# Kernel tuning notes

Measured on AMD Instinct MI355X. Metric: run time of the kernel, lower is better.

The kernel has to match this reference:

```python
import jax, jax.numpy as jnp
import numpy as np

B, T, C = 2, 2048, 1024
H = 16
HD = C // H  # head_dim = 64
SCALE = HD ** -0.5

def setup_inputs() -> dict:
    key = jax.random.key(0)
    ks = jax.random.split(key, 5)
    s = 1.0 / np.sqrt(C)
    return {
        "x": jax.random.normal(ks[0], (B, T, C), dtype=jnp.float32),
        "Wq": jax.random.normal(ks[1], (C, C), dtype=jnp.float32) * s,
        "Wk": jax.random.normal(ks[2], (C, C), dtype=jnp.float32) * s,
        "Wv": jax.random.normal(ks[3], (C, C), dtype=jnp.float32) * s,
        "Wp": jax.random.normal(ks[4], (C, C), dtype=jnp.float32) * s,
        "bp": jnp.zeros((C,), dtype=jnp.float32),
    }

def reference(x, Wq, Wk, Wv, Wp, bp):
    b, t, c = x.shape
    # QKV projections (no bias, qkv_bias=False) -> [B,T,H,HD]
    q = (x @ Wq).reshape(b, t, H, HD)
    k = (x @ Wk).reshape(b, t, H, HD)
    v = (x @ Wv).reshape(b, t, H, HD)
    # scores [B,H,T,T]
    scores = jnp.einsum("bqhd,bkhd->bhqk", q, k) * SCALE
    causal = jnp.tril(jnp.ones((t, t), dtype=bool))
    scores = jnp.where(causal, scores, -jnp.inf)
    attn = jax.nn.softmax(scores, axis=-1)  # dropout = identity (eval mode)
    out = jnp.einsum("bhqk,bkhd->bqhd", attn, v).reshape(b, t, c)
    return out @ Wp + bp
```

## Files before the change

### kernel.cpp

```cpp
#include <hip/hip_runtime.h>


typedef __attribute__((ext_vector_type(8))) short shortx8;
typedef __attribute__((ext_vector_type(4))) short shortx4;
typedef __attribute__((ext_vector_type(8))) unsigned short ushortx8;
typedef __attribute__((ext_vector_type(4))) float f32x4;
typedef __attribute__((ext_vector_type(16))) float f32x16;
typedef __attribute__((ext_vector_type(2))) unsigned uintx2;

#define MFMA16(a, b, c) __builtin_amdgcn_mfma_f32_16x16x32_bf16((a), (b), (c), 0, 0, 0)
#define MFMA32(a, b, c) __builtin_amdgcn_mfma_f32_32x32x16_bf16((a), (b), (c), 0, 0, 0)

#define SC_L2E 0.18033688011112042f

__device__ __forceinline__ unsigned short f2bf(float f) {
  union { float f; unsigned u; } v; v.f = f;
  unsigned r = v.u + 0x7fffu + ((v.u >> 16) & 1u);
  return (unsigned short)(r >> 16);
}

__device__ __forceinline__ unsigned cvtpk(float a, float b) {
  unsigned r;
  asm("v_cvt_pk_bf16_f32 %0, %1, %2" : "=v"(r) : "v"(a), "v"(b));
  return r;
}

__device__ __forceinline__ float fexp2(float x) {
#if __has_builtin(__builtin_amdgcn_exp2f)
  return __builtin_amdgcn_exp2f(x);
#else
  return exp2f(x);
#endif
}

__device__ __forceinline__ uintx2 plswap(unsigned a, unsigned b) {
#if __has_builtin(__builtin_amdgcn_permlane32_swap)
  return __builtin_amdgcn_permlane32_swap(a, b, false, false);
#else
  asm volatile("v_permlane32_swap_b32 %0, %1" : "+v"(a), "+v"(b));
  uintx2 r; r[0] = a; r[1] = b; return r;
#endif
}

__device__ __forceinline__ float partner32(float x, int hi) {
  unsigned u = __builtin_bit_cast(unsigned, x);
  uintx2 r = plswap(u, u);
  return __builtin_bit_cast(float, hi ? r[0] : r[1]);
}

__device__ __forceinline__ float max3(float a, float b, float c) {
  return fmaxf(fmaxf(a, b), c);
}

__device__ __forceinline__ void gload16(const void* g, void* l) {
  __builtin_amdgcn_global_load_lds(
      (const __attribute__((address_space(1))) void*)g,
      (__attribute__((address_space(3))) void*)l, 16, 0, 0);
}

__global__ __launch_bounds__(256) void cvt_x(const float* __restrict__ x,
                                             unsigned short* __restrict__ xb, int n4) {
  int i = blockIdx.x * 256 + threadIdx.x;
  if (i < n4) {
    float4 v = ((const float4*)x)[i];
    unsigned short* o = xb + (size_t)i * 4;
    o[0] = f2bf(v.x); o[1] = f2bf(v.y); o[2] = f2bf(v.z); o[3] = f2bf(v.w);
  }
}

__global__ __launch_bounds__(256) void transpose_w4(
    const float* __restrict__ Wq, const float* __restrict__ Wk,
    const float* __restrict__ Wv, const float* __restrict__ Wp,
    unsigned short* __restrict__ wqkvT, unsigned short* __restrict__ wpT) {
  __shared__ float tile[32][33];
  const int zi = blockIdx.z;
  const float* src = (zi == 0) ? Wq : (zi == 1) ? Wk : (zi == 2) ? Wv : Wp;
  unsigned short* dst = (zi == 3) ? wpT : wqkvT + (size_t)zi * 1048576;
  const int bx = blockIdx.x * 32, by = blockIdx.y * 32;
  const int tx = threadIdx.x & 31, ty = threadIdx.x >> 5;
  #pragma unroll
  for (int i = 0; i < 32; i += 8)
    tile[ty + i][tx] = src[(size_t)(by + ty + i) * 1024 + bx + tx];
  __syncthreads();
  #pragma unroll
  for (int i = 0; i < 32; i += 8)
    dst[(size_t)(bx + ty + i) * 1024 + by + tx] = f2bf(tile[tx][ty + i]);
}

__global__ __launch_bounds__(256) void gemm_bt(
    const unsigned short* __restrict__ A, const unsigned short* __restrict__ BT,
    unsigned short* __restrict__ Cb, float* __restrict__ Cf,
    const float* __restrict__ bias, int M, int N, int K,
    float qscale, int scale_cols, unsigned short* __restrict__ vTo) {
  __shared__ unsigned short As[3][4096];
  __shared__ unsigned short Bs[3][4096];
  const int tid = threadIdx.x;
  const int lane = tid & 63, w = tid >> 6;
  const int wr = w >> 1, wc = w & 1;
  const int brow = blockIdx.y << 7, bcol = blockIdx.x << 7;

  f32x4 z = {0.f, 0.f, 0.f, 0.f};
  f32x4 acc[4][4];
  #pragma unroll
  for (int m = 0; m < 4; ++m)
    #pragma unroll
    for (int n = 0; n < 4; ++n) acc[m][n] = z;

  const int srow = tid >> 2;
  const int scol = (tid & 3) << 3;
  const unsigned short* Ap = A + (size_t)(brow + srow) * K + scol;
  const unsigned short* Bp = BT + (size_t)(bcol + srow) * K + scol;
  const size_t rowK64 = (size_t)64 * K;

  #define GSTAGE(k0_, bi_)                                   \
    do {                                                     \
      unsigned short* AsW = &As[bi_][w * 512];               \
      unsigned short* BsW = &Bs[bi_][w * 512];               \
      gload16(Ap + (k0_), AsW);                              \
      gload16(Ap + rowK64 + (k0_), AsW + 2048);              \
      gload16(Bp + (k0_), BsW);                              \
      gload16(Bp + rowK64 + (k0_), BsW + 2048);              \
    } while (0)

  const int koff = (lane >> 4) << 3;
  const int ar = (wr << 6) + (lane & 15);
  const int br = (wc << 6) + (lane & 15);
  const int nt = K >> 5;
  int cur = 0;
  GSTAGE(0, 0);
  for (int t = 0; t < nt; ++t) {
    const int nxt = (cur + 1 == 3) ? 0 : cur + 1;
    if (t + 1 < nt) {
      GSTAGE((size_t)(t + 1) << 5, nxt);
      asm volatile("s_waitcnt vmcnt(4)" ::: "memory");
    } else {
      asm volatile("s_waitcnt vmcnt(0)" ::: "memory");
    }
    __builtin_amdgcn_sched_barrier(0);
    __builtin_amdgcn_s_barrier();
    __builtin_amdgcn_sched_barrier(0);
    shortx8 af[4], bf[4];
    #pragma unroll
    for (int m = 0; m < 4; ++m) af[m] = *(const shortx8*)&As[cur][(ar + m * 16) * 32 + koff];
    #pragma unroll
    for (int n = 0; n < 4; ++n) bf[n] = *(const shortx8*)&Bs[cur][(br + n * 16) * 32 + koff];
    #pragma unroll
    for (int m = 0; m < 4; ++m)
      #pragma unroll
      for (int n = 0; n < 4; ++n) acc[m][n] = MFMA16(af[m], bf[n], acc[m][n]);
    asm volatile("s_waitcnt lgkmcnt(0)" ::: "memory");
    __builtin_amdgcn_sched_barrier(0);
    cur = nxt;
  }
  #undef GSTAGE

  const int r0 = (lane >> 4) << 2;
  const int c0 = lane & 15;
  if (Cb) {
    if (vTo && bcol >= 2048) {
      #pragma unroll
      for (int m = 0; m < 4; ++m)
        #pragma unroll
        for (int n = 0; n < 4; ++n) {
          const int dp = bcol - 2048 + (wc << 6) + n * 16 + c0;
          const size_t rowb = brow + (wr << 6) + m * 16 + r0;
          uint2 u;
          u.x = cvtpk(acc[m][n][0], acc[m][n][1]);
          u.y = cvtpk(acc[m][n][2], acc[m][n][3]);
          *(uint2*)&vTo[(size_t)dp * 4096 + rowb] = u;
        }
    } else {
      #pragma unroll
      for (int m = 0; m < 4; ++m)
        #pragma unroll
        for (int n = 0; n < 4; ++n)
          #pragma unroll
          for (int j = 0; j < 4; ++j) {
            const size_t row = brow + (wr << 6) + m * 16 + r0 + j;
            const size_t col = bcol + (wc << 6) + n * 16 + c0;
            float v = acc[m][n][j];
            if ((int)col < scale_cols) v *= qscale;
            Cb[row * N + col] = f2bf(v);
          }
    }
  } else {
    #pragma unroll
    for (int m = 0; m < 4; ++m)
      #pragma unroll
      for (int n = 0; n < 4; ++n)
        #pragma unroll
        for (int j = 0; j < 4; ++j) {
          const size_t row = brow + (wr << 6) + m * 16 + r0 + j;
          const size_t col = bcol + (wc << 6) + n * 16 + c0;
          Cf[row * N + col] = acc[m][n][j] + bias[col];
        }
  }
}


__global__ __launch_bounds__(256, 4) void attn_fwd(
    const unsigned short* __restrict__ qkv, const unsigned short* __restrict__ vT,
    unsigned short* __restrict__ att) {
  __shared__ unsigned short sh[4][4096];

  const int tid = threadIdx.x;
  const int lane = tid & 63;
  const int p = tid >> 6;
  const int stream = blockIdx.x;
  const int h = stream & 15, b = stream >> 4;
  const int qb = 63 - (int)blockIdx.y;
  const int ql = lane & 31;
  const int hi = lane >> 5;
  const int q = qb * 32 + ql;

  shortx8 qf[4];
  {
    const unsigned short* qp = qkv + ((size_t)(b * 2048 + q)) * 3072 + h * 64 + 8 * hi;
    #pragma unroll
    for (int kc = 0; kc < 4; ++kc) qf[kc] = *(const shortx8*)(qp + 16 * kc);
  }

  f32x16 z16;
  #pragma unroll
  for (int i = 0; i < 16; ++i) z16[i] = 0.f;
  f32x16 accO0 = z16, accO1 = z16;
  float m_run = -__builtin_inff(), l_run = 0.f;

  const unsigned short* kb[4];
  const unsigned short* vb[4];
  #pragma unroll
  for (int i = 0; i < 4; ++i) {
    const int krow = 8 * i + (lane >> 3);
    const int kcl = (lane & 7) ^ (((krow >> 1) ^ (krow >> 4)) & 7);
    kb[i] = qkv + ((size_t)(b * 2048 + krow)) * 3072 + 1024 + h * 64 + 8 * kcl;
    const int vrow = 16 * i + (lane >> 2);
    const int vcl = (lane & 3) ^ (((vrow >> 1) ^ (vrow >> 3)) & 3);
    vb[i] = vT + ((size_t)(h * 64 + vrow)) * 4096 + b * 2048 + 8 * vcl;
  }
  const int rs8 = ((ql >> 1) ^ (ql >> 4)) & 7;
  const int rs4 = ((ql >> 1) ^ (ql >> 3)) & 3;

  unsigned short* Kl = &sh[p][0];
  unsigned short* Vl = &sh[p][2048];

  #define STAGE(t_)                                                        \
    do {                                                                   \
      _Pragma("unroll")                                                    \
      for (int i = 0; i < 4; ++i)                                          \
        gload16(kb[i] + (size_t)(t_) * 32 * 3072, Kl + i * 512);           \
      _Pragma("unroll")                                                    \
      for (int i = 0; i < 4; ++i)                                          \
        gload16(vb[i] + (t_) * 32, Vl + i * 512);                          \
    } while (0)

  if (p <= qb) STAGE(p);
  for (int t = p; t <= qb; t += 4) {
    asm volatile("s_waitcnt vmcnt(4)" ::: "memory");
    __builtin_amdgcn_sched_barrier(0);
    shortx8 kf[4];
    #pragma unroll
    for (int kc = 0; kc < 4; ++kc)
      kf[kc] = *(const shortx8*)&Kl[ql * 64 + 8 * ((2 * kc + hi) ^ rs8)];
    asm volatile("s_waitcnt lgkmcnt(0)" ::: "memory");
    __builtin_amdgcn_sched_barrier(0);

    __builtin_amdgcn_s_setprio(1);
    f32x16 s = z16;
    #pragma unroll
    for (int kc = 0; kc < 4; ++kc) s = MFMA32(kf[kc], qf[kc], s);
    __builtin_amdgcn_s_setprio(0);

    asm volatile("s_waitcnt vmcnt(0)" ::: "memory");
    __builtin_amdgcn_sched_barrier(0);
    shortx8 vf[2][2];
    #pragma unroll
    for (int dh = 0; dh < 2; ++dh)
      #pragma unroll
      for (int ks = 0; ks < 2; ++ks)
        vf[dh][ks] = *(const shortx8*)&Vl[(32 * dh + ql) * 32 + 8 * ((2 * ks + hi) ^ rs4)];
    asm volatile("s_waitcnt lgkmcnt(0)" ::: "memory");
    __builtin_amdgcn_sched_barrier(0);

    if (t + 4 <= qb) STAGE(t + 4);

    if (t == qb) {
      #pragma unroll
      for (int r = 0; r < 16; ++r) {
        const int kvl = (r & 3) + 8 * (r >> 2) + 4 * hi;
        if (kvl > ql) s[r] = -__builtin_inff();
      }
    }

    float t0 = max3(s[0], s[1], s[2]);
    float t1 = max3(s[3], s[4], s[5]);
    float t2 = max3(s[6], s[7], s[8]);
    float t3 = max3(s[9], s[10], s[11]);
    float t4 = max3(s[12], s[13], s[14]);
    float mx = fmaxf(max3(t0, t1, t2), max3(t3, t4, s[15]));
    mx = fmaxf(mx, partner32(mx, hi));

    if (!__all(mx <= m_run + 8.0f)) {
      const float nm = fmaxf(m_run, mx);
      const float alpha = fexp2(m_run - nm);
      l_run *= alpha;
      #pragma unroll
      for (int r = 0; r < 16; ++r) { accO0[r] *= alpha; accO1[r] *= alpha; }
      m_run = nm;
    }

    #pragma unroll
    for (int r = 0; r < 16; ++r) s[r] = fexp2(s[r] - m_run);
    float a8[8], a4[4];
    #pragma unroll
    for (int i = 0; i < 8; ++i) a8[i] = s[2 * i] + s[2 * i + 1];
    #pragma unroll
    for (int i = 0; i < 4; ++i) a4[i] = a8[2 * i] + a8[2 * i + 1];
    float rsum = (a4[0] + a4[1]) + (a4[2] + a4[3]);
    rsum += partner32(rsum, hi);
    l_run += rsum;

    unsigned wv[8];
    #pragma unroll
    for (int i = 0; i < 8; ++i) wv[i] = cvtpk(s[2 * i], s[2 * i + 1]);
    __builtin_amdgcn_s_setprio(1);
    #pragma unroll
    for (int ss = 0; ss < 2; ++ss) {
      uintx2 r02 = plswap(wv[4 * ss], wv[4 * ss + 2]);
      uintx2 r13 = plswap(wv[4 * ss + 1], wv[4 * ss + 3]);
      union { unsigned u[4]; shortx8 s8; } pb;
      pb.u[0] = r02[0];
      pb.u[1] = r13[0];
      pb.u[2] = r02[1];
      pb.u[3] = r13[1];
      accO0 = MFMA32(vf[0][ss], pb.s8, accO0);
      accO1 = MFMA32(vf[1][ss], pb.s8, accO1);
    }
    __builtin_amdgcn_s_setprio(0);
  }
  #undef STAGE

  float* fb = (float*)&sh[0][0];
  #define DUMP(slot_)                                                          \
    do {                                                                       \
      float* ob = fb + (slot_) * 2048;                                         \
      _Pragma("unroll")                                                        \
      for (int rg = 0; rg < 4; ++rg) {                                         \
        f32x4 v0 = {accO0[4 * rg], accO0[4 * rg + 1],                          \
                    accO0[4 * rg + 2], accO0[4 * rg + 3]};                     \
        f32x4 v1 = {accO1[4 * rg], accO1[4 * rg + 1],                          \
                    accO1[4 * rg + 2], accO1[4 * rg + 3]};                     \
        *(f32x4*)&ob[(rg * 64 + lane) * 4] = v0;                               \
        *(f32x4*)&ob[((4 + rg) * 64 + lane) * 4] = v1;                         \
      }                                                                        \
      fb[4096 + (slot_) * 128 + lane] = m_run;                                 \
      fb[4096 + (slot_) * 128 + 64 + lane] = l_run;                            \
    } while (0)
  #define MERGE(slot_)                                                         \
    do {                                                                       \
      const float m2 = fb[4096 + (slot_) * 128 + lane];                        \
      const float l2 = fb[4096 + (slot_) * 128 + 64 + lane];                   \
      if (m2 != -__builtin_inff()) {                                           \
        float* ob = fb + (slot_) * 2048;                                       \
        const float mf = fmaxf(m_run, m2);                                     \
        const float a1 = fexp2(m_run - mf);                                    \
        const float a2 = fexp2(m2 - mf);                                       \
        _Pragma("unroll")                                                      \
        for (int rg = 0; rg < 4; ++rg) {                                       \
          f32x4 p0 = *(const f32x4*)&ob[(rg * 64 + lane) * 4];                 \
          f32x4 p1 = *(const f32x4*)&ob[((4 + rg) * 64 + lane) * 4];           \
          _Pragma("unroll")                                                    \
          for (int j = 0; j < 4; ++j) {                                        \
            accO0[4 * rg + j] = accO0[4 * rg + j] * a1 + p0[j] * a2;           \
            accO1[4 * rg + j] = accO1[4 * rg + j] * a1 + p1[j] * a2;           \
          }                                                                    \
        }                                                                      \
        l_run = l_run * a1 + l2 * a2;                                          \
        m_run = mf;                                                            \
      }                                                                        \
    } while (0)

  __syncthreads();
  if (p == 1) DUMP(0);
  if (p == 3) DUMP(1);
  __syncthreads();
  if (p == 0) MERGE(0);
  if (p == 2) MERGE(1);
  __syncthreads();
  if (p == 2) DUMP(0);
  __syncthreads();
  if (p == 0) {
    MERGE(0);
    const float inv = 1.f / l_run;
    unsigned short* op = att + ((size_t)(b * 2048 + q)) * 1024 + h * 64;
    #pragma unroll
    for (int rq = 0; rq < 4; ++rq) {
      shortx4 o0, o1;
      #pragma unroll
      for (int j = 0; j < 4; ++j) {
        o0[j] = (short)f2bf(accO0[4 * rq + j] * inv);
        o1[j] = (short)f2bf(accO1[4 * rq + j] * inv);
      }
      *(shortx4*)&op[8 * rq + 4 * hi] = o0;
      *(shortx4*)&op[32 + 8 * rq + 4 * hi] = o1;
    }
  }
  #undef DUMP
  #undef MERGE
}

extern "C" void kernel_launch(void* const* d_in, const int* in_sizes, int n_in,
                              void* d_out, int out_size, void* d_ws, size_t ws_size,
                              hipStream_t stream) {
  const float* x  = (const float*)d_in[0];
  const float* Wq = (const float*)d_in[1];
  const float* Wk = (const float*)d_in[2];
  const float* Wv = (const float*)d_in[3];
  const float* Wp = (const float*)d_in[4];
  const float* bp = (const float*)d_in[5];

  char* ws = (char*)d_ws;
  unsigned short* xb    = (unsigned short*)(ws);
  unsigned short* wqkvT = (unsigned short*)(ws + (size_t)8  * 1048576);
  unsigned short* wpT   = (unsigned short*)(ws + (size_t)14 * 1048576);
  unsigned short* qkv   = (unsigned short*)(ws + (size_t)16 * 1048576);
  unsigned short* vT    = (unsigned short*)(ws + (size_t)40 * 1048576);
  unsigned short* att   = (unsigned short*)(ws + (size_t)48 * 1048576);

  cvt_x<<<dim3(4096), dim3(256), 0, stream>>>(x, xb, 1048576);
  transpose_w4<<<dim3(32, 32, 4), dim3(256), 0, stream>>>(Wq, Wk, Wv, Wp, wqkvT, wpT);
  gemm_bt<<<dim3(24, 32), dim3(256), 0, stream>>>(xb, wqkvT, qkv, nullptr, nullptr,
                                                  4096, 3072, 1024, SC_L2E, 1024, vT);
  attn_fwd<<<dim3(32, 64), dim3(256), 0, stream>>>(qkv, vT, att);
  gemm_bt<<<dim3(8, 32), dim3(256), 0, stream>>>(att, wpT, nullptr, (float*)d_out, bp,
                                                 4096, 1024, 1024, 0.f, 0, nullptr);
}
```

Before: 107.8 us.

## Shrink GEMM blocks to 128x64 tiles with two waves and double buffering

The bf16 GEMM changes from 128x128 tiles computed by four waves to 128x64 tiles computed by two waves. This doubles the grid for both the QKV and output projections, and the smaller output-projection launch gains more blocks to spread across CUs. The LDS pipeline drops from triple to double buffering, with an extra barrier per k-step so a buffer is not overwritten while still being read. The trade-off is less operand reuse per block, more global traffic for the A operand, and extra synchronisation per k-step.

```diff
diff --git a/kernel.cpp b/kernel.cpp
--- a/kernel.cpp
+++ b/kernel.cpp
@@ -87,17 +87,16 @@
     dst[(size_t)(bx + ty + i) * 1024 + by + tx] = f2bf(tile[tx][ty + i]);
 }
 
-__global__ __launch_bounds__(256) void gemm_bt(
+__global__ __launch_bounds__(128) void gemm_bt(
     const unsigned short* __restrict__ A, const unsigned short* __restrict__ BT,
     unsigned short* __restrict__ Cb, float* __restrict__ Cf,
     const float* __restrict__ bias, int M, int N, int K,
     float qscale, int scale_cols, unsigned short* __restrict__ vTo) {
-  __shared__ unsigned short As[3][4096];
-  __shared__ unsigned short Bs[3][4096];
+  __shared__ unsigned short As[2][4096];
+  __shared__ unsigned short Bs[2][2048];
   const int tid = threadIdx.x;
   const int lane = tid & 63, w = tid >> 6;
-  const int wr = w >> 1, wc = w & 1;
-  const int brow = blockIdx.y << 7, bcol = blockIdx.x << 7;
+  const int brow = blockIdx.y << 7, bcol = blockIdx.x << 6;
 
   f32x4 z = {0.f, 0.f, 0.f, 0.f};
   f32x4 acc[4][4];
@@ -110,29 +109,30 @@
   const int scol = (tid & 3) << 3;
   const unsigned short* Ap = A + (size_t)(brow + srow) * K + scol;
   const unsigned short* Bp = BT + (size_t)(bcol + srow) * K + scol;
-  const size_t rowK64 = (size_t)64 * K;
-
-  #define GSTAGE(k0_, bi_)                                   \
-    do {                                                     \
-      unsigned short* AsW = &As[bi_][w * 512];               \
-      unsigned short* BsW = &Bs[bi_][w * 512];               \
-      gload16(Ap + (k0_), AsW);                              \
-      gload16(Ap + rowK64 + (k0_), AsW + 2048);              \
-      gload16(Bp + (k0_), BsW);                              \
-      gload16(Bp + rowK64 + (k0_), BsW + 2048);              \
+  const size_t rowK32 = (size_t)32 * K;
+
+  #define GSTAGE(k0_, bi_)                                            \
+    do {                                                              \
+      _Pragma("unroll")                                               \
+      for (int i = 0; i < 4; ++i)                                     \
+        gload16(Ap + (size_t)i * rowK32 + (k0_),                      \
+                &As[bi_][i * 1024 + (w << 9)]);                       \
+      _Pragma("unroll")                                               \
+      for (int i = 0; i < 2; ++i)                                     \
+        gload16(Bp + (size_t)i * rowK32 + (k0_),                      \
+                &Bs[bi_][i * 1024 + (w << 9)]);                       \
     } while (0)
 
   const int koff = (lane >> 4) << 3;
-  const int ar = (wr << 6) + (lane & 15);
-  const int br = (wc << 6) + (lane & 15);
+  const int ar = (w << 6) + (lane & 15);
+  const int br = (lane & 15);
   const int nt = K >> 5;
-  int cur = 0;
+  int bufi = 0;
   GSTAGE(0, 0);
   for (int t = 0; t < nt; ++t) {
-    const int nxt = (cur + 1 == 3) ? 0 : cur + 1;
     if (t + 1 < nt) {
-      GSTAGE((size_t)(t + 1) << 5, nxt);
-      asm volatile("s_waitcnt vmcnt(4)" ::: "memory");
+      GSTAGE((size_t)(t + 1) << 5, bufi ^ 1);
+      asm volatile("s_waitcnt vmcnt(6)" ::: "memory");
     } else {
       asm volatile("s_waitcnt vmcnt(0)" ::: "memory");
     }
@@ -141,16 +141,18 @@
     __builtin_amdgcn_sched_barrier(0);
     shortx8 af[4], bf[4];
     #pragma unroll
-    for (int m = 0; m < 4; ++m) af[m] = *(const shortx8*)&As[cur][(ar + m * 16) * 32 + koff];
-    #pragma unroll
-    for (int n = 0; n < 4; ++n) bf[n] = *(const shortx8*)&Bs[cur][(br + n * 16) * 32 + koff];
+    for (int m = 0; m < 4; ++m) af[m] = *(const shortx8*)&As[bufi][(ar + m * 16) * 32 + koff];
+    #pragma unroll
+    for (int n = 0; n < 4; ++n) bf[n] = *(const shortx8*)&Bs[bufi][(br + n * 16) * 32 + koff];
     #pragma unroll
     for (int m = 0; m < 4; ++m)
       #pragma unroll
       for (int n = 0; n < 4; ++n) acc[m][n] = MFMA16(af[m], bf[n], acc[m][n]);
     asm volatile("s_waitcnt lgkmcnt(0)" ::: "memory");
     __builtin_amdgcn_sched_barrier(0);
-    cur = nxt;
+    __builtin_amdgcn_s_barrier();
+    __builtin_amdgcn_sched_barrier(0);
+    bufi ^= 1;
   }
   #undef GSTAGE
 
@@ -162,8 +164,8 @@
       for (int m = 0; m < 4; ++m)
         #pragma unroll
         for (int n = 0; n < 4; ++n) {
-          const int dp = bcol - 2048 + (wc << 6) + n * 16 + c0;
-          const size_t rowb = brow + (wr << 6) + m * 16 + r0;
+          const int dp = bcol - 2048 + n * 16 + c0;
+          const size_t rowb = brow + (w << 6) + m * 16 + r0;
           uint2 u;
           u.x = cvtpk(acc[m][n][0], acc[m][n][1]);
           u.y = cvtpk(acc[m][n][2], acc[m][n][3]);
@@ -176,8 +178,8 @@
         for (int n = 0; n < 4; ++n)
           #pragma unroll
           for (int j = 0; j < 4; ++j) {
-            const size_t row = brow + (wr << 6) + m * 16 + r0 + j;
-            const size_t col = bcol + (wc << 6) + n * 16 + c0;
+            const size_t row = brow + (w << 6) + m * 16 + r0 + j;
+            const size_t col = bcol + n * 16 + c0;
             float v = acc[m][n][j];
             if ((int)col < scale_cols) v *= qscale;
             Cb[row * N + col] = f2bf(v);
@@ -190,8 +192,8 @@
       for (int n = 0; n < 4; ++n)
         #pragma unroll
         for (int j = 0; j < 4; ++j) {
-          const size_t row = brow + (wr << 6) + m * 16 + r0 + j;
-          const size_t col = bcol + (wc << 6) + n * 16 + c0;
+          const size_t row = brow + (w << 6) + m * 16 + r0 + j;
+          const size_t col = bcol + n * 16 + c0;
           Cf[row * N + col] = acc[m][n][j] + bias[col];
         }
   }
@@ -428,9 +430,9 @@
 
   cvt_x<<<dim3(4096), dim3(256), 0, stream>>>(x, xb, 1048576);
   transpose_w4<<<dim3(32, 32, 4), dim3(256), 0, stream>>>(Wq, Wk, Wv, Wp, wqkvT, wpT);
-  gemm_bt<<<dim3(24, 32), dim3(256), 0, stream>>>(xb, wqkvT, qkv, nullptr, nullptr,
+  gemm_bt<<<dim3(48, 32), dim3(128), 0, stream>>>(xb, wqkvT, qkv, nullptr, nullptr,
                                                   4096, 3072, 1024, SC_L2E, 1024, vT);
   attn_fwd<<<dim3(32, 64), dim3(256), 0, stream>>>(qkv, vT, att);
-  gemm_bt<<<dim3(8, 32), dim3(256), 0, stream>>>(att, wpT, nullptr, (float*)d_out, bp,
-                                                 4096, 1024, 1024, 0.f, 0, nullptr);
-}
+  gemm_bt<<<dim3(16, 32), dim3(128), 0, stream>>>(att, wpT, nullptr, (float*)d_out, bp,
+                                                  4096, 1024, 1024, 0.f, 0, nullptr);
+}
```

New measurement: 118.7 us. +10.0%, slower.

## Process two 32-row query tiles per attention block to reuse staged K/V

Applied to the files above, without the earlier changes.

Each attention workgroup now handles 64 query rows as two 32-row sub-tiles (A and B) that share every K/V tile staged in LDS, which halves the grid and the global K/V traffic per query. Sub-tile A is skipped on the final KV tile, and each sub-tile gets its own causal mask. Launch bounds drop from 4 to 3 waves per SIMD to make room for the doubled accumulators and Q fragments. The cost is lower occupancy, twice as many cross-wave merge trees at the end, and fewer blocks to balance the causal workload.

```diff
diff --git a/kernel.cpp b/kernel.cpp
--- a/kernel.cpp
+++ b/kernel.cpp
@@ -198,7 +198,7 @@
 }
 
 
-__global__ __launch_bounds__(256, 4) void attn_fwd(
+__global__ __launch_bounds__(256, 3) void attn_fwd(
     const unsigned short* __restrict__ qkv, const unsigned short* __restrict__ vT,
     unsigned short* __restrict__ att) {
   __shared__ unsigned short sh[4][4096];
@@ -208,23 +208,30 @@
   const int p = tid >> 6;
   const int stream = blockIdx.x;
   const int h = stream & 15, b = stream >> 4;
-  const int qb = 63 - (int)blockIdx.y;
+  const int qb = 31 - (int)blockIdx.y;
   const int ql = lane & 31;
   const int hi = lane >> 5;
-  const int q = qb * 32 + ql;
-
-  shortx8 qf[4];
+  const int qA = qb * 64 + ql;
+  const int qB = qA + 32;
+
+  shortx8 qfA[4], qfB[4];
   {
-    const unsigned short* qp = qkv + ((size_t)(b * 2048 + q)) * 3072 + h * 64 + 8 * hi;
-    #pragma unroll
-    for (int kc = 0; kc < 4; ++kc) qf[kc] = *(const shortx8*)(qp + 16 * kc);
+    const unsigned short* qpA = qkv + ((size_t)(b * 2048 + qA)) * 3072 + h * 64 + 8 * hi;
+    const unsigned short* qpB = qkv + ((size_t)(b * 2048 + qB)) * 3072 + h * 64 + 8 * hi;
+    #pragma unroll
+    for (int kc = 0; kc < 4; ++kc) {
+      qfA[kc] = *(const shortx8*)(qpA + 16 * kc);
+      qfB[kc] = *(const shortx8*)(qpB + 16 * kc);
+    }
   }
 
   f32x16 z16;
   #pragma unroll
   for (int i = 0; i < 16; ++i) z16[i] = 0.f;
-  f32x16 accO0 = z16, accO1 = z16;
-  float m_run = -__builtin_inff(), l_run = 0.f;
+  f32x16 accA0 = z16, accA1 = z16;
+  f32x16 accB0 = z16, accB1 = z16;
+  float mA = -__builtin_inff(), lA = 0.f;
+  float mB = -__builtin_inff(), lB = 0.f;
 
   const unsigned short* kb[4];
   const unsigned short* vb[4];
@@ -253,8 +260,57 @@
         gload16(vb[i] + (t_) * 32, Vl + i * 512);                          \
     } while (0)
 
-  if (p <= qb) STAGE(p);
-  for (int t = p; t <= qb; t += 4) {
+  #define SMAX(s_, mr_, lr_, A0_, A1_, wv_)                                \
+    do {                                                                   \
+      float t0 = max3(s_[0], s_[1], s_[2]);                                \
+      float t1 = max3(s_[3], s_[4], s_[5]);                                \
+      float t2 = max3(s_[6], s_[7], s_[8]);                                \
+      float t3 = max3(s_[9], s_[10], s_[11]);                              \
+      float t4 = max3(s_[12], s_[13], s_[14]);                             \
+      float mx = fmaxf(max3(t0, t1, t2), max3(t3, t4, s_[15]));            \
+      mx = fmaxf(mx, partner32(mx, hi));                                   \
+      if (!__all(mx <= (mr_) + 8.0f)) {                                    \
+        const float nm = fmaxf(mr_, mx);                                   \
+        const float alpha = fexp2((mr_) - nm);                             \
+        (lr_) *= alpha;                                                    \
+        _Pragma("unroll")                                                  \
+        for (int r = 0; r < 16; ++r) { A0_[r] *= alpha; A1_[r] *= alpha; } \
+        (mr_) = nm;                                                        \
+      }                                                                    \
+      _Pragma("unroll")                                                    \
+      for (int r = 0; r < 16; ++r) s_[r] = fexp2(s_[r] - (mr_));           \
+      float a8[8], a4[4];                                                  \
+      _Pragma("unroll")                                                    \
+      for (int i = 0; i < 8; ++i) a8[i] = s_[2 * i] + s_[2 * i + 1];       \
+      _Pragma("unroll")                                                    \
+      for (int i = 0; i < 4; ++i) a4[i] = a8[2 * i] + a8[2 * i + 1];       \
+      float rsum = (a4[0] + a4[1]) + (a4[2] + a4[3]);                      \
+      rsum += partner32(rsum, hi);                                         \
+      (lr_) += rsum;                                                       \
+      _Pragma("unroll")                                                    \
+      for (int i = 0; i < 8; ++i) wv_[i] = cvtpk(s_[2 * i], s_[2 * i + 1]);\
+    } while (0)
+
+  #define PV(wv_, A0_, A1_)                                                \
+    do {                                                                   \
+      _Pragma("unroll")                                                    \
+      for (int ss = 0; ss < 2; ++ss) {                                     \
+        uintx2 r02 = plswap(wv_[4 * ss], wv_[4 * ss + 2]);                 \
+        uintx2 r13 = plswap(wv_[4 * ss + 1], wv_[4 * ss + 3]);             \
+        union { unsigned u[4]; shortx8 s8; } pb;                           \
+        pb.u[0] = r02[0];                                                  \
+        pb.u[1] = r13[0];                                                  \
+        pb.u[2] = r02[1];                                                  \
+        pb.u[3] = r13[1];                                                  \
+        A0_ = MFMA32(vf[0][ss], pb.s8, A0_);                               \
+        A1_ = MFMA32(vf[1][ss], pb.s8, A1_);                               \
+      }                                                                    \
+    } while (0)
+
+  const int tmax = 2 * qb + 1;
+  if (p <= tmax) STAGE(p);
+  for (int t = p; t <= tmax; t += 4) {
+    const bool actA = (t <= 2 * qb);
     asm volatile("s_waitcnt vmcnt(4)" ::: "memory");
     __builtin_amdgcn_sched_barrier(0);
     shortx8 kf[4];
@@ -264,10 +320,27 @@
     asm volatile("s_waitcnt lgkmcnt(0)" ::: "memory");
     __builtin_amdgcn_sched_barrier(0);
 
+    unsigned wvA[8];
+    if (actA) {
+      __builtin_amdgcn_s_setprio(1);
+      f32x16 sA = z16;
+      #pragma unroll
+      for (int kc = 0; kc < 4; ++kc) sA = MFMA32(kf[kc], qfA[kc], sA);
+      __builtin_amdgcn_s_setprio(0);
+      if (t == 2 * qb) {
+        #pragma unroll
+        for (int r = 0; r < 16; ++r) {
+          const int kvl = (r & 3) + 8 * (r >> 2) + 4 * hi;
+          if (kvl > ql) sA[r] = -__builtin_inff();
+        }
+      }
+      SMAX(sA, mA, lA, accA0, accA1, wvA);
+    }
+
     __builtin_amdgcn_s_setprio(1);
-    f32x16 s = z16;
-    #pragma unroll
-    for (int kc = 0; kc < 4; ++kc) s = MFMA32(kf[kc], qf[kc], s);
+    f32x16 sB = z16;
+    #pragma unroll
+    for (int kc = 0; kc < 4; ++kc) sB = MFMA32(kf[kc], qfB[kc], sB);
     __builtin_amdgcn_s_setprio(0);
 
     asm volatile("s_waitcnt vmcnt(0)" ::: "memory");
@@ -281,88 +354,47 @@
     asm volatile("s_waitcnt lgkmcnt(0)" ::: "memory");
     __builtin_amdgcn_sched_barrier(0);
 
-    if (t + 4 <= qb) STAGE(t + 4);
-
-    if (t == qb) {
+    if (t + 4 <= tmax) STAGE(t + 4);
+
+    if (t == tmax) {
       #pragma unroll
       for (int r = 0; r < 16; ++r) {
         const int kvl = (r & 3) + 8 * (r >> 2) + 4 * hi;
-        if (kvl > ql) s[r] = -__builtin_inff();
+        if (kvl > ql) sB[r] = -__builtin_inff();
       }
     }
-
-    float t0 = max3(s[0], s[1], s[2]);
-    float t1 = max3(s[3], s[4], s[5]);
-    float t2 = max3(s[6], s[7], s[8]);
-    float t3 = max3(s[9], s[10], s[11]);
-    float t4 = max3(s[12], s[13], s[14]);
-    float mx = fmaxf(max3(t0, t1, t2), max3(t3, t4, s[15]));
-    mx = fmaxf(mx, partner32(mx, hi));
-
-    if (!__all(mx <= m_run + 8.0f)) {
-      const float nm = fmaxf(m_run, mx);
-      const float alpha = fexp2(m_run - nm);
-      l_run *= alpha;
-      #pragma unroll
-      for (int r = 0; r < 16; ++r) { accO0[r] *= alpha; accO1[r] *= alpha; }
-      m_run = nm;
-    }
-
-    #pragma unroll
-    for (int r = 0; r < 16; ++r) s[r] = fexp2(s[r] - m_run);
-    float a8[8], a4[4];
-    #pragma unroll
-    for (int i = 0; i < 8; ++i) a8[i] = s[2 * i] + s[2 * i + 1];
-    #pragma unroll
-    for (int i = 0; i < 4; ++i) a4[i] = a8[2 * i] + a8[2 * i + 1];
-    float rsum = (a4[0] + a4[1]) + (a4[2] + a4[3]);
-    rsum += partner32(rsum, hi);
-    l_run += rsum;
-
-    unsigned wv[8];
-    #pragma unroll
-    for (int i = 0; i < 8; ++i) wv[i] = cvtpk(s[2 * i], s[2 * i + 1]);
+    unsigned wvB[8];
+    SMAX(sB, mB, lB, accB0, accB1, wvB);
+
     __builtin_amdgcn_s_setprio(1);
-    #pragma unroll
-    for (int ss = 0; ss < 2; ++ss) {
-      uintx2 r02 = plswap(wv[4 * ss], wv[4 * ss + 2]);
-      uintx2 r13 = plswap(wv[4 * ss + 1], wv[4 * ss + 3]);
-      union { unsigned u[4]; shortx8 s8; } pb;
-      pb.u[0] = r02[0];
-      pb.u[1] = r13[0];
-      pb.u[2] = r02[1];
-      pb.u[3] = r13[1];
-      accO0 = MFMA32(vf[0][ss], pb.s8, accO0);
-      accO1 = MFMA32(vf[1][ss], pb.s8, accO1);
-    }
+    if (actA) PV(wvA, accA0, accA1);
+    PV(wvB, accB0, accB1);
     __builtin_amdgcn_s_setprio(0);
   }
   #undef STAGE
 
   float* fb = (float*)&sh[0][0];
-  #define DUMP(slot_)                                                          \
+  #define DUMP(slot_, A0_, A1_, mr_, lr_)                                      \
     do {                                                                       \
       float* ob = fb + (slot_) * 2048;                                         \
       _Pragma("unroll")                                                        \
       for (int rg = 0; rg < 4; ++rg) {                                         \
-        f32x4 v0 = {accO0[4 * rg], accO0[4 * rg + 1],                          \
-                    accO0[4 * rg + 2], accO0[4 * rg + 3]};                     \
-        f32x4 v1 = {accO1[4 * rg], accO1[4 * rg + 1],                          \
-                    accO1[4 * rg + 2], accO1[4 * rg + 3]};                     \
+        f32x4 v0 = {A0_[4 * rg], A0_[4 * rg + 1], A0_[4 * rg + 2], A0_[4 * rg + 3]}; \
+        f32x4 v1 = {A1_[4 * rg], A1_[4 * rg + 1], A1_[4 * rg + 2], A1_[4 * rg + 3]}; \
         *(f32x4*)&ob[(rg * 64 + lane) * 4] = v0;                               \
         *(f32x4*)&ob[((4 + rg) * 64 + lane) * 4] = v1;                         \
       }                                                                        \
-      fb[4096 + (slot_) * 128 + lane] = m_run;                                 \
-      fb[4096 + (slot_) * 128 + 64 + lane] = l_run;                            \
-    } while (0)
-  #define MERGE(slot_)                                                         \
+      fb[4096 + (slot_) * 128 + lane] = (mr_);                                 \
+      fb[4096 + (slot_) * 128 + 64 + lane] = (lr_);                            \
+    } while (0)
+  #define MERGE(slot_, A0_, A1_, mr_, lr_)                                     \
     do {                                                                       \
       const float m2 = fb[4096 + (slot_) * 128 + lane];                        \
       const float l2 = fb[4096 + (slot_) * 128 + 64 + lane];                   \
       if (m2 != -__builtin_inff()) {                                           \
         float* ob = fb + (slot_) * 2048;                                       \
-        const float mf = fmaxf(m_run, m2);                                     \
-        const float a1 = fexp2(m_run - mf);                                    \
+        const float mf = fmaxf(mr_, m2);                                       \
+        const float a1 = fexp2((mr_) - mf);                                    \
         const float a2 = fexp2(m2 - mf);                                       \
         _Pragma("unroll")                                                      \
         for (int rg = 0; rg < 4; ++rg) {                                       \
@@ -370,42 +402,50 @@
           f32x4 p1 = *(const f32x4*)&ob[((4 + rg) * 64 + lane) * 4];           \
           _Pragma("unroll")                                                    \
           for (int j = 0; j < 4; ++j) {                                        \
-            accO0[4 * rg + j] = accO0[4 * rg + j] * a1 + p0[j] * a2;           \
-            accO1[4 * rg + j] = accO1[4 * rg + j] * a1 + p1[j] * a2;           \
+            A0_[4 * rg + j] = A0_[4 * rg + j] * a1 + p0[j] * a2;               \
+            A1_[4 * rg + j] = A1_[4 * rg + j] * a1 + p1[j] * a2;               \
           }                                                                    \
         }                                                                      \
-        l_run = l_run * a1 + l2 * a2;                                          \
-        m_run = mf;                                                            \
+        (lr_) = (lr_) * a1 + l2 * a2;                                          \
+        (mr_) = mf;                                                            \
       }                                                                        \
     } while (0)
-
-  __syncthreads();
-  if (p == 1) DUMP(0);
-  if (p == 3) DUMP(1);
-  __syncthreads();
-  if (p == 0) MERGE(0);
-  if (p == 2) MERGE(1);
-  __syncthreads();
-  if (p == 2) DUMP(0);
-  __syncthreads();
-  if (p == 0) {
-    MERGE(0);
-    const float inv = 1.f / l_run;
-    unsigned short* op = att + ((size_t)(b * 2048 + q)) * 1024 + h * 64;
-    #pragma unroll
-    for (int rq = 0; rq < 4; ++rq) {
-      shortx4 o0, o1;
-      #pragma unroll
-      for (int j = 0; j < 4; ++j) {
-        o0[j] = (short)f2bf(accO0[4 * rq + j] * inv);
-        o1[j] = (short)f2bf(accO1[4 * rq + j] * inv);
-      }
-      *(shortx4*)&op[8 * rq + 4 * hi] = o0;
-      *(shortx4*)&op[32 + 8 * rq + 4 * hi] = o1;
-    }
-  }
+  #define TREE(A0_, A1_, mr_, lr_, qrow_)                                      \
+    do {                                                                       \
+      __syncthreads();                                                         \
+      if (p == 1) DUMP(0, A0_, A1_, mr_, lr_);                                 \
+      if (p == 3) DUMP(1, A0_, A1_, mr_, lr_);                                 \
+      __syncthreads();                                                         \
+      if (p == 0) MERGE(0, A0_, A1_, mr_, lr_);                                \
+      if (p == 2) MERGE(1, A0_, A1_, mr_, lr_);                                \
+      __syncthreads();                                                         \
+      if (p == 2) DUMP(0, A0_, A1_, mr_, lr_);                                 \
+      __syncthreads();                                                         \
+      if (p == 0) {                                                            \
+        MERGE(0, A0_, A1_, mr_, lr_);                                          \
+        const float inv = 1.f / (lr_);                                         \
+        unsigned short* op = att + ((size_t)(b * 2048 + (qrow_))) * 1024 + h * 64; \
+        _Pragma("unroll")                                                      \
+        for (int rq = 0; rq < 4; ++rq) {                                       \
+          shortx4 o0, o1;                                                      \
+          _Pragma("unroll")                                                    \
+          for (int j = 0; j < 4; ++j) {                                        \
+            o0[j] = (short)f2bf(A0_[4 * rq + j] * inv);                        \
+            o1[j] = (short)f2bf(A1_[4 * rq + j] * inv);                        \
+          }                                                                    \
+          *(shortx4*)&op[8 * rq + 4 * hi] = o0;                                \
+          *(shortx4*)&op[32 + 8 * rq + 4 * hi] = o1;                           \
+        }                                                                      \
+      }                                                                        \
+    } while (0)
+
+  TREE(accA0, accA1, mA, lA, qA);
+  TREE(accB0, accB1, mB, lB, qB);
   #undef DUMP
   #undef MERGE
+  #undef TREE
+  #undef SMAX
+  #undef PV
 }
 
 extern "C" void kernel_launch(void* const* d_in, const int* in_sizes, int n_in,
@@ -430,7 +470,7 @@
   transpose_w4<<<dim3(32, 32, 4), dim3(256), 0, stream>>>(Wq, Wk, Wv, Wp, wqkvT, wpT);
   gemm_bt<<<dim3(24, 32), dim3(256), 0, stream>>>(xb, wqkvT, qkv, nullptr, nullptr,
                                                   4096, 3072, 1024, SC_L2E, 1024, vT);
-  attn_fwd<<<dim3(32, 64), dim3(256), 0, stream>>>(qkv, vT, att);
+  attn_fwd<<<dim3(32, 32), dim3(256), 0, stream>>>(qkv, vT, att);
   gemm_bt<<<dim3(8, 32), dim3(256), 0, stream>>>(att, wpT, nullptr, (float*)d_out, bp,
                                                  4096, 1024, 1024, 0.f, 0, nullptr);
 }
```

Measured after the change: 111.8 us. 3.7% more time.
